# Kernel optimization log

Measured on AMD Instinct MI355X. Metric: run time of the kernel, lower is better.

## Reference

```python
import jax, jax.numpy as jnp
import numpy as np

SPLIT_SIZE = 64
EPS_NORM = 1e-12  # torch F.normalize eps
EPS_DIV = 1e-8


def _l2_normalize(x):
    n = jnp.linalg.norm(x, axis=-1, keepdims=True)
    return x / jnp.maximum(n, EPS_NORM)


def setup_inputs() -> dict:
    key = jax.random.key(0)
    current_split_idx = 1023
    seq_len = (current_split_idx + 1) * SPLIT_SIZE  # 65536
    d_model = 1024
    batch = 2
    embeddings = jax.random.normal(key, (batch, seq_len, d_model), dtype=jnp.float32)
    return {"embeddings": embeddings, "current_split_idx": current_split_idx, "k": 7}


def reference(embeddings, current_split_idx, k):
    B, S, d = embeddings.shape
    n_avail = current_split_idx + 1
    req = n_avail * SPLIT_SIZE
    if current_split_idx == 0:
        indices = jnp.full((B, 1), current_split_idx, dtype=jnp.int64)
        weights = jnp.ones((B, 1), dtype=embeddings.dtype)
        return indices, weights
    # static pad/truncate to exactly n_avail splits
    if S < req:
        emb = jnp.pad(embeddings, ((0, 0), (0, req - S), (0, 0)))
    else:
        emb = embeddings[:, :req, :]
    splits = emb.reshape(B, n_avail, SPLIT_SIZE, d)
    cur = _l2_normalize(splits[:, current_split_idx])          # [B, ss, d]
    prev = _l2_normalize(splits[:, :current_split_idx])        # [B, n_prev, ss, d]
    # sims[b,n,q,p] = <cur[b,q], prev[b,n,p]>; MaxSim: max over prev tokens p, sum over query tokens q
    sims = jnp.einsum('bqd,bnpd->bnqp', cur, prev)
    scores = sims.max(axis=-1).sum(axis=-1)                     # [B, n_prev]
    k_actual = min(k, current_split_idx)
    top_scores, top_indices = jax.lax.top_k(scores, k_actual)
    max_score = top_scores.max(axis=1, keepdims=True)
    normalized = top_scores / (max_score + EPS_DIV)
    all_indices = jnp.concatenate(
        [top_indices.astype(jnp.int64),
         jnp.full((B, 1), current_split_idx, dtype=jnp.int64)], axis=1)
    all_weights = jnp.concatenate(
        [normalized, jnp.ones((B, 1), dtype=normalized.dtype)], axis=1)
    return all_indices, all_weights
```

## Files before the change

### kernel.cpp

```cpp
#include <hip/hip_runtime.h>
#include <math.h>

#define D_MODEL   1024
#define SPLIT     64
#define B_BATCH   2
#define SEQ       65536
#define CSI       1023
#define NPREV     1023
#define KSEL      7
#define RCAND     32

typedef __attribute__((ext_vector_type(8)))  short short8;
typedef __attribute__((ext_vector_type(16))) float floatx16;

static __device__ __forceinline__ ushort f2bf_rne(float x) {
    union { float f; unsigned u; } v; v.f = x;
    unsigned r = v.u + 0x7fffu + ((v.u >> 16) & 1u);
    return (ushort)(r >> 16);
}

#define RS  72
#define TSZ (SPLIT * RS)

__global__ __launch_bounds__(256) void score_mfma(const float* __restrict__ emb,
                                                  float* __restrict__ scores) {
    const int n = blockIdx.x, b = blockIdx.y;
    const int t = threadIdx.x;
    const int lane = t & 63, wave = t >> 6;

    __shared__ ushort tiles[2 * TSZ];
    __shared__ float sA[SPLIT], sB[SPLIT], ivA[SPLIT], ivB[SPLIT];
    ushort* At = tiles;
    ushort* Bt = tiles + TSZ;
    float* red = (float*)tiles;

    const float* curB = emb + ((size_t)b * SEQ + (size_t)CSI * SPLIT) * D_MODEL;
    const float* prvB = emb + ((size_t)b * SEQ + (size_t)n   * SPLIT) * D_MODEL;

    floatx16 acc[2][2] = {};
    float pA[4] = {0.f, 0.f, 0.f, 0.f}, pB[4] = {0.f, 0.f, 0.f, 0.f};

    const int sr = t >> 4;
    const int sc = (t & 15) << 2;

    const int rm  = lane & 31;
    const int kq  = (lane >> 5) << 3;
    const int kb  = wave << 4;
    const int fo  = rm * RS + kb + kq;
    const short8* fA0 = (const short8*)(At + fo);
    const short8* fA1 = (const short8*)(At + fo + 32 * RS);
    const short8* fB0 = (const short8*)(Bt + fo);
    const short8* fB1 = (const short8*)(Bt + fo + 32 * RS);

    for (int c = 0; c < 16; ++c) {
        const int k0 = c << 6;
        __syncthreads();
        #pragma unroll
        for (int it = 0; it < 4; ++it) {
            const int r = sr + (it << 4);
            const float4 av = *(const float4*)(curB + (size_t)r * D_MODEL + k0 + sc);
            const float4 bv = *(const float4*)(prvB + (size_t)r * D_MODEL + k0 + sc);
            pA[it] = fmaf(av.x, av.x, fmaf(av.y, av.y, fmaf(av.z, av.z, fmaf(av.w, av.w, pA[it]))));
            pB[it] = fmaf(bv.x, bv.x, fmaf(bv.y, bv.y, fmaf(bv.z, bv.z, fmaf(bv.w, bv.w, pB[it]))));
            ushort4 h;
            h.x = f2bf_rne(av.x); h.y = f2bf_rne(av.y);
            h.z = f2bf_rne(av.z); h.w = f2bf_rne(av.w);
            *(ushort4*)(At + r * RS + sc) = h;
            h.x = f2bf_rne(bv.x); h.y = f2bf_rne(bv.y);
            h.z = f2bf_rne(bv.z); h.w = f2bf_rne(bv.w);
            *(ushort4*)(Bt + r * RS + sc) = h;
        }
        __syncthreads();

        const short8 a0 = *fA0, a1 = *fA1;
        const short8 b0 = *fB0, b1 = *fB1;

        acc[0][0] = __builtin_amdgcn_mfma_f32_32x32x16_bf16(a0, b0, acc[0][0], 0, 0, 0);
        acc[0][1] = __builtin_amdgcn_mfma_f32_32x32x16_bf16(a0, b1, acc[0][1], 0, 0, 0);
        acc[1][0] = __builtin_amdgcn_mfma_f32_32x32x16_bf16(a1, b0, acc[1][0], 0, 0, 0);
        acc[1][1] = __builtin_amdgcn_mfma_f32_32x32x16_bf16(a1, b1, acc[1][1], 0, 0, 0);
    }

    #pragma unroll
    for (int m = 1; m < 16; m <<= 1) {
        #pragma unroll
        for (int it = 0; it < 4; ++it) {
            pA[it] += __shfl_xor(pA[it], m, 64);
            pB[it] += __shfl_xor(pB[it], m, 64);
        }
    }
    if ((t & 15) == 0) {
        #pragma unroll
        for (int it = 0; it < 4; ++it) { sA[sr + (it << 4)] = pA[it]; sB[sr + (it << 4)] = pB[it]; }
    }
    __syncthreads();
    if (t < 64)        ivB[t]      = 1.f / fmaxf(sqrtf(sB[t]),      1e-12f);
    else if (t < 128)  ivA[t - 64] = 1.f / fmaxf(sqrtf(sA[t - 64]), 1e-12f);
    __syncthreads();

    const int cc = lane & 31;
    const int rquad = (lane >> 5) << 2;
    for (int ph = 0; ph < 4; ++ph) {
        if (wave == ph) {
            #pragma unroll
            for (int mt = 0; mt < 2; ++mt)
            #pragma unroll
            for (int nt = 0; nt < 2; ++nt) {
                #pragma unroll
                for (int r = 0; r < 16; ++r) {
                    const int row = mt * 32 + (r & 3) + ((r >> 2) << 3) + rquad;
                    const int col = nt * 32 + cc;
                    const float v = acc[mt][nt][r];
                    if (ph == 0) red[row * 65 + col] = v;
                    else         red[row * 65 + col] += v;
                }
            }
        }
        __syncthreads();
    }

    if (t < 64) {
        const float* rr = red + t * 65;
        float m = -INFINITY;
        for (int p = 0; p < 64; ++p) m = fmaxf(m, rr[p] * ivB[p]);
        float v = m * ivA[t];
        #pragma unroll
        for (int o = 1; o < 64; o <<= 1) v += __shfl_xor(v, o, 64);
        if (t == 0) scores[(size_t)b * NPREV + n] = v;
    }
}

__global__ __launch_bounds__(256) void select_top(const float* __restrict__ scores,
                                                  int* __restrict__ sel) {
    const int b = blockIdx.x, t = threadIdx.x;
    __shared__ float sv[NPREV];
    __shared__ float wv[4]; __shared__ int wi[4];
    for (int i = t; i < NPREV; i += 256) sv[i] = scores[(size_t)b * NPREV + i];
    __syncthreads();
    for (int r = 0; r < RCAND; ++r) {
        float bv = -INFINITY; int bi = 0x7fffffff;
        for (int i = t; i < NPREV; i += 256) {
            const float v = sv[i];
            if (v > bv || (v == bv && i < bi)) { bv = v; bi = i; }
        }
        #pragma unroll
        for (int o = 1; o < 64; o <<= 1) {
            const float ov = __shfl_xor(bv, o, 64); const int oi = __shfl_xor(bi, o, 64);
            if (ov > bv || (ov == bv && oi < bi)) { bv = ov; bi = oi; }
        }
        if ((t & 63) == 0) { wv[t >> 6] = bv; wi[t >> 6] = bi; }
        __syncthreads();
        if (t == 0) {
            float fv = wv[0]; int fi = wi[0];
            for (int w = 1; w < 4; ++w)
                if (wv[w] > fv || (wv[w] == fv && wi[w] < fi)) { fv = wv[w]; fi = wi[w]; }
            sel[b * RCAND + r] = fi;
            sv[fi] = -INFINITY;
        }
        __syncthreads();
    }
}

#define BK      64
#define LDS_STR 68

__global__ __launch_bounds__(256) void rescore_kernel(const float* __restrict__ emb,
                                                      const int* __restrict__ sel,
                                                      float* __restrict__ resc) {
    const int j   = blockIdx.x;
    const int b   = blockIdx.y;
    const int n   = sel[b * RCAND + j];
    const int tid = threadIdx.x;
    const int tx  = tid & 15;
    const int ty  = tid >> 4;
    const int q0  = ty * 4;
    const int p0  = tx * 4;

    __shared__ float As[BK][LDS_STR];
    __shared__ float Bs[BK][LDS_STR];
    __shared__ float invA[SPLIT];
    __shared__ float invB[SPLIT];
    __shared__ float rowmax[SPLIT];

    const float* curBase = emb + ((size_t)b * SEQ + (size_t)CSI * SPLIT) * D_MODEL;
    const float* prvBase = emb + ((size_t)b * SEQ + (size_t)n   * SPLIT) * D_MODEL;

    float acc[4][4] = {};
    float ssq = 0.f;

    const int lr = tid >> 4;
    const int lc = (tid & 15) * 4;

    for (int k0 = 0; k0 < D_MODEL; k0 += BK) {
        __syncthreads();
        #pragma unroll
        for (int it = 0; it < 4; ++it) {
            const int r = lr + 16 * it;
            const float4 a  = *(const float4*)(curBase + (size_t)r * D_MODEL + k0 + lc);
            const float4 bv = *(const float4*)(prvBase + (size_t)r * D_MODEL + k0 + lc);
            As[lc + 0][r] = a.x;  As[lc + 1][r] = a.y;  As[lc + 2][r] = a.z;  As[lc + 3][r] = a.w;
            Bs[lc + 0][r] = bv.x; Bs[lc + 1][r] = bv.y; Bs[lc + 2][r] = bv.z; Bs[lc + 3][r] = bv.w;
        }
        __syncthreads();

        if (tid < 64) {
            const int p = tid;
            #pragma unroll 8
            for (int kk = 0; kk < BK; ++kk) { const float v = Bs[kk][p]; ssq = fmaf(v, v, ssq); }
        } else if (tid < 128) {
            const int q = tid - 64;
            #pragma unroll 8
            for (int kk = 0; kk < BK; ++kk) { const float v = As[kk][q]; ssq = fmaf(v, v, ssq); }
        }

        #pragma unroll 8
        for (int kk = 0; kk < BK; ++kk) {
            const float4 a  = *(const float4*)&As[kk][q0];
            const float4 bv = *(const float4*)&Bs[kk][p0];
            const float av[4]  = {a.x, a.y, a.z, a.w};
            const float bvv[4] = {bv.x, bv.y, bv.z, bv.w};
            #pragma unroll
            for (int i = 0; i < 4; ++i)
                #pragma unroll
                for (int jj = 0; jj < 4; ++jj)
                    acc[i][jj] = fmaf(av[i], bvv[jj], acc[i][jj]);
        }
    }

    __syncthreads();
    if (tid < 64)       invB[tid]      = 1.f / fmaxf(sqrtf(ssq), 1e-12f);
    else if (tid < 128) invA[tid - 64] = 1.f / fmaxf(sqrtf(ssq), 1e-12f);
    __syncthreads();

    float ibv[4];
    #pragma unroll
    for (int jj = 0; jj < 4; ++jj) ibv[jj] = invB[p0 + jj];

    float rmax[4];
    #pragma unroll
    for (int i = 0; i < 4; ++i) {
        float m = -INFINITY;
        #pragma unroll
        for (int jj = 0; jj < 4; ++jj) m = fmaxf(m, acc[i][jj] * ibv[jj]);
        rmax[i] = m * invA[q0 + i];
    }
    #pragma unroll
    for (int off = 1; off < 16; off <<= 1) {
        #pragma unroll
        for (int i = 0; i < 4; ++i)
            rmax[i] = fmaxf(rmax[i], __shfl_xor(rmax[i], off, 64));
    }
    if (tx == 0) {
        #pragma unroll
        for (int i = 0; i < 4; ++i) rowmax[q0 + i] = rmax[i];
    }
    __syncthreads();

    if (tid < 64) {
        float v = rowmax[tid];
        #pragma unroll
        for (int off = 1; off < 64; off <<= 1) v += __shfl_xor(v, off, 64);
        if (tid == 0) resc[b * RCAND + j] = v;
    }
}

__global__ void final_topk(const int* __restrict__ sel, const float* __restrict__ resc,
                           float* __restrict__ out) {
    const int t = threadIdx.x;
    const int b = t >> 5, j = t & 31;
    float v  = resc[b * RCAND + j];
    const int idx = sel[b * RCAND + j];

    float outv = 0.f, maxv = 0.f; int outi = 0;
    for (int r = 0; r < KSEL; ++r) {
        float bv = v; int bi = idx;
        #pragma unroll
        for (int o = 1; o < 32; o <<= 1) {
            const float ov = __shfl_xor(bv, o, 64); const int oi = __shfl_xor(bi, o, 64);
            if (ov > bv || (ov == bv && oi < bi)) { bv = ov; bi = oi; }
        }
        if (r == 0) maxv = bv;
        if (j == r) { outv = bv; outi = bi; }
        if (idx == bi) v = -INFINITY;
    }
    if (j < KSEL) {
        out[b * (KSEL + 1) + j]                        = (float)outi;
        out[B_BATCH * (KSEL + 1) + b * (KSEL + 1) + j] = outv / (maxv + 1e-8f);
    }
    if (j == 31) {
        out[b * (KSEL + 1) + KSEL]                        = (float)CSI;
        out[B_BATCH * (KSEL + 1) + b * (KSEL + 1) + KSEL] = 1.0f;
    }
}

extern "C" void kernel_launch(void* const* d_in, const int* in_sizes, int n_in,
                              void* d_out, int out_size, void* d_ws, size_t ws_size,
                              hipStream_t stream) {
    const float* emb = (const float*)d_in[0];
    float* out = (float*)d_out;

    float* scores = (float*)d_ws;
    int*   sel    = (int*)((char*)d_ws + 2048 * sizeof(float));
    float* resc   = (float*)((char*)d_ws + 2048 * sizeof(float) + 64 * sizeof(int));

    dim3 g1(NPREV, B_BATCH);
    score_mfma<<<g1, 256, 0, stream>>>(emb, scores);
    select_top<<<B_BATCH, 256, 0, stream>>>(scores, sel);
    dim3 g3(RCAND, B_BATCH);
    rescore_kernel<<<g3, 256, 0, stream>>>(emb, sel, resc);
    final_topk<<<1, 64, 0, stream>>>(sel, resc, out);
}
```

Before: 820.6 us.

## Precompute bf16 current split and norms once; single-wave-per-batch top-k selection

Adds a small pre-kernel that converts the current split to bf16 and computes its inverse L2 norms once per batch, so each of the 2046 score blocks loads half-size bf16 data for A and skips its norm and conversion work. The selection kernel is rewritten to keep one wave per batch, with each lane's candidates held in registers, which removes the shared-memory and __syncthreads rounds. This costs an extra kernel launch and a small workspace buffer. The per-lane scan now breaks ties by the first index that lane encounters, and the wave reduction still picks the lowest index.

```diff
diff --git a/kernel.cpp b/kernel.cpp
--- a/kernel.cpp
+++ b/kernel.cpp
@@ -19,26 +19,52 @@
     return (ushort)(r >> 16);
 }
 
+__global__ __launch_bounds__(256) void cvt_cur(const float* __restrict__ emb,
+                                               ushort* __restrict__ curbf,
+                                               float* __restrict__ curnorm) {
+    const int b = blockIdx.x;
+    const int t = threadIdx.x;
+    const int row = t >> 2;
+    const int q   = t & 3;
+    const float* src = emb + ((size_t)b * SEQ + (size_t)CSI * SPLIT + row) * D_MODEL + q * 256;
+    ushort* dst = curbf + ((size_t)b * SPLIT + row) * D_MODEL + q * 256;
+    float ssq = 0.f;
+    #pragma unroll 8
+    for (int i = 0; i < 64; ++i) {
+        const float4 v = *(const float4*)(src + i * 4);
+        ssq = fmaf(v.x, v.x, fmaf(v.y, v.y, fmaf(v.z, v.z, fmaf(v.w, v.w, ssq))));
+        ushort4 h;
+        h.x = f2bf_rne(v.x); h.y = f2bf_rne(v.y);
+        h.z = f2bf_rne(v.z); h.w = f2bf_rne(v.w);
+        *(ushort4*)(dst + i * 4) = h;
+    }
+    ssq += __shfl_xor(ssq, 1, 64);
+    ssq += __shfl_xor(ssq, 2, 64);
+    if (q == 0) curnorm[b * SPLIT + row] = 1.f / fmaxf(sqrtf(ssq), 1e-12f);
+}
+
 #define RS  72
 #define TSZ (SPLIT * RS)
 
 __global__ __launch_bounds__(256) void score_mfma(const float* __restrict__ emb,
+                                                  const ushort* __restrict__ curbf,
+                                                  const float* __restrict__ curnorm,
                                                   float* __restrict__ scores) {
     const int n = blockIdx.x, b = blockIdx.y;
     const int t = threadIdx.x;
     const int lane = t & 63, wave = t >> 6;
 
     __shared__ ushort tiles[2 * TSZ];
-    __shared__ float sA[SPLIT], sB[SPLIT], ivA[SPLIT], ivB[SPLIT];
+    __shared__ float sB[SPLIT], ivB[SPLIT];
     ushort* At = tiles;
     ushort* Bt = tiles + TSZ;
     float* red = (float*)tiles;
 
-    const float* curB = emb + ((size_t)b * SEQ + (size_t)CSI * SPLIT) * D_MODEL;
-    const float* prvB = emb + ((size_t)b * SEQ + (size_t)n   * SPLIT) * D_MODEL;
+    const ushort* curA = curbf + (size_t)b * SPLIT * D_MODEL;
+    const float*  prvB = emb + ((size_t)b * SEQ + (size_t)n * SPLIT) * D_MODEL;
 
     floatx16 acc[2][2] = {};
-    float pA[4] = {0.f, 0.f, 0.f, 0.f}, pB[4] = {0.f, 0.f, 0.f, 0.f};
+    float pB[4] = {0.f, 0.f, 0.f, 0.f};
 
     const int sr = t >> 4;
     const int sc = (t & 15) << 2;
@@ -58,14 +84,11 @@
         #pragma unroll
         for (int it = 0; it < 4; ++it) {
             const int r = sr + (it << 4);
-            const float4 av = *(const float4*)(curB + (size_t)r * D_MODEL + k0 + sc);
+            *(ushort4*)(At + r * RS + sc) =
+                *(const ushort4*)(curA + (size_t)r * D_MODEL + k0 + sc);
             const float4 bv = *(const float4*)(prvB + (size_t)r * D_MODEL + k0 + sc);
-            pA[it] = fmaf(av.x, av.x, fmaf(av.y, av.y, fmaf(av.z, av.z, fmaf(av.w, av.w, pA[it]))));
             pB[it] = fmaf(bv.x, bv.x, fmaf(bv.y, bv.y, fmaf(bv.z, bv.z, fmaf(bv.w, bv.w, pB[it]))));
             ushort4 h;
-            h.x = f2bf_rne(av.x); h.y = f2bf_rne(av.y);
-            h.z = f2bf_rne(av.z); h.w = f2bf_rne(av.w);
-            *(ushort4*)(At + r * RS + sc) = h;
             h.x = f2bf_rne(bv.x); h.y = f2bf_rne(bv.y);
             h.z = f2bf_rne(bv.z); h.w = f2bf_rne(bv.w);
             *(ushort4*)(Bt + r * RS + sc) = h;
@@ -84,18 +107,14 @@
     #pragma unroll
     for (int m = 1; m < 16; m <<= 1) {
         #pragma unroll
-        for (int it = 0; it < 4; ++it) {
-            pA[it] += __shfl_xor(pA[it], m, 64);
-            pB[it] += __shfl_xor(pB[it], m, 64);
-        }
+        for (int it = 0; it < 4; ++it) pB[it] += __shfl_xor(pB[it], m, 64);
     }
     if ((t & 15) == 0) {
         #pragma unroll
-        for (int it = 0; it < 4; ++it) { sA[sr + (it << 4)] = pA[it]; sB[sr + (it << 4)] = pB[it]; }
-    }
-    __syncthreads();
-    if (t < 64)        ivB[t]      = 1.f / fmaxf(sqrtf(sB[t]),      1e-12f);
-    else if (t < 128)  ivA[t - 64] = 1.f / fmaxf(sqrtf(sA[t - 64]), 1e-12f);
+        for (int it = 0; it < 4; ++it) sB[sr + (it << 4)] = pB[it];
+    }
+    __syncthreads();
+    if (t < 64) ivB[t] = 1.f / fmaxf(sqrtf(sB[t]), 1e-12f);
     __syncthreads();
 
     const int cc = lane & 31;
@@ -120,44 +139,44 @@
     }
 
     if (t < 64) {
+        const float myIvA = curnorm[b * SPLIT + t];
         const float* rr = red + t * 65;
         float m = -INFINITY;
         for (int p = 0; p < 64; ++p) m = fmaxf(m, rr[p] * ivB[p]);
-        float v = m * ivA[t];
+        float v = m * myIvA;
         #pragma unroll
         for (int o = 1; o < 64; o <<= 1) v += __shfl_xor(v, o, 64);
         if (t == 0) scores[(size_t)b * NPREV + n] = v;
     }
 }
 
-__global__ __launch_bounds__(256) void select_top(const float* __restrict__ scores,
-                                                  int* __restrict__ sel) {
-    const int b = blockIdx.x, t = threadIdx.x;
-    __shared__ float sv[NPREV];
-    __shared__ float wv[4]; __shared__ int wi[4];
-    for (int i = t; i < NPREV; i += 256) sv[i] = scores[(size_t)b * NPREV + i];
-    __syncthreads();
+__global__ void select_top(const float* __restrict__ scores,
+                           int* __restrict__ sel) {
+    const int t = threadIdx.x;
+    const int b = t >> 6, lane = t & 63;
+    float v[16];
+    #pragma unroll
+    for (int i = 0; i < 16; ++i) {
+        const int idx = lane + (i << 6);
+        v[i] = (idx < NPREV) ? scores[(size_t)b * NPREV + idx] : -INFINITY;
+    }
     for (int r = 0; r < RCAND; ++r) {
         float bv = -INFINITY; int bi = 0x7fffffff;
-        for (int i = t; i < NPREV; i += 256) {
-            const float v = sv[i];
-            if (v > bv || (v == bv && i < bi)) { bv = v; bi = i; }
+        #pragma unroll
+        for (int i = 0; i < 16; ++i) {
+            const int idx = lane + (i << 6);
+            if (v[i] > bv) { bv = v[i]; bi = idx; }
         }
         #pragma unroll
         for (int o = 1; o < 64; o <<= 1) {
-            const float ov = __shfl_xor(bv, o, 64); const int oi = __shfl_xor(bi, o, 64);
+            const float ov = __shfl_xor(bv, o, 64);
+            const int   oi = __shfl_xor(bi, o, 64);
             if (ov > bv || (ov == bv && oi < bi)) { bv = ov; bi = oi; }
         }
-        if ((t & 63) == 0) { wv[t >> 6] = bv; wi[t >> 6] = bi; }
-        __syncthreads();
-        if (t == 0) {
-            float fv = wv[0]; int fi = wi[0];
-            for (int w = 1; w < 4; ++w)
-                if (wv[w] > fv || (wv[w] == fv && wi[w] < fi)) { fv = wv[w]; fi = wi[w]; }
-            sel[b * RCAND + r] = fi;
-            sv[fi] = -INFINITY;
-        }
-        __syncthreads();
+        if (lane == 0) sel[b * RCAND + r] = bi;
+        #pragma unroll
+        for (int i = 0; i < 16; ++i)
+            if (bi == lane + (i << 6)) v[i] = -INFINITY;
     }
 }
 
@@ -299,13 +318,17 @@
     const float* emb = (const float*)d_in[0];
     float* out = (float*)d_out;
 
-    float* scores = (float*)d_ws;
-    int*   sel    = (int*)((char*)d_ws + 2048 * sizeof(float));
-    float* resc   = (float*)((char*)d_ws + 2048 * sizeof(float) + 64 * sizeof(int));
-
+    char* ws = (char*)d_ws;
+    float*  scores  = (float*)ws;
+    int*    sel     = (int*)(ws + (16 << 10));
+    float*  resc    = (float*)(ws + (17 << 10));
+    float*  curnorm = (float*)(ws + (18 << 10));
+    ushort* curbf   = (ushort*)(ws + (20 << 10));
+
+    cvt_cur<<<B_BATCH, 256, 0, stream>>>(emb, curbf, curnorm);
     dim3 g1(NPREV, B_BATCH);
-    score_mfma<<<g1, 256, 0, stream>>>(emb, scores);
-    select_top<<<B_BATCH, 256, 0, stream>>>(scores, sel);
+    score_mfma<<<g1, 256, 0, stream>>>(emb, curbf, curnorm, scores);
+    select_top<<<1, 128, 0, stream>>>(scores, sel);
     dim3 g3(RCAND, B_BATCH);
     rescore_kernel<<<g3, 256, 0, stream>>>(emb, sel, resc);
     final_topk<<<1, 64, 0, stream>>>(sel, resc, out);
```

New measurement: 811.0 us. Within noise of the previous version (-1.2%).
